# Performance work log

Hardware: AMD Instinct MI355X
Metric: run time of the kernel (lower is better)

Reference implementation:

```python
import jax, jax.numpy as jnp
import numpy as np
from jax import lax

L_TAU = 0.8
NUM_TIME = 20
B, H, W = 128, 64, 64
FLAT = 6 * 27 * 27  # 4374 features after conv(k=10)->55x55 and maxpool2 -> 27x27

def setup_inputs() -> dict:
    key = jax.random.key(0)
    k1, k2, k3, k4, k5, k6 = jax.random.split(key, 6)
    x = jax.random.uniform(k1, (B, H * W, NUM_TIME), dtype=jnp.float32)
    y = jax.random.randint(k2, (B,), 0, 2, dtype=jnp.int64)
    Wc = jax.random.normal(k3, (6, 1, 10, 10), dtype=jnp.float32) * 0.1  # OIHW
    bc = jnp.zeros((6,), dtype=jnp.float32)
    W2 = jax.random.normal(k4, (FLAT, 2), dtype=jnp.float32) * (1.0 / np.sqrt(FLAT))
    b2 = jnp.zeros((2,), dtype=jnp.float32)
    return {"x": x, "y": y, "Wc": Wc, "bc": bc, "W2": W2, "b2": b2}

def _maxpool2(a):
    return lax.reduce_window(a, -jnp.inf, lax.max,
                             (1, 1, 2, 2), (1, 1, 2, 2), 'VALID')

def _snu_forward(x, Wc, bc, W2, b2):
    xt = jnp.transpose(x, (2, 0, 1)).reshape(NUM_TIME, B, 1, H, W)  # [T,B,1,64,64]
    s1 = jnp.zeros((B, 6, 55, 55), jnp.float32); y1 = jnp.zeros_like(s1)
    s2 = jnp.zeros((B, 2), jnp.float32);        y2 = jnp.zeros_like(s2)

    def step(carry, x_t):
        s1, y1, s2, y2 = carry
        c = lax.conv_general_dilated(x_t, Wc, (1, 1), 'VALID',
                                     dimension_numbers=('NCHW', 'OIHW', 'NCHW'))
        # SNU state: s = relu(conv(x) + l_tau * s * (1 - y)); emission: y = sigmoid(s + b)
        s1 = jax.nn.relu(c + L_TAU * s1 * (1.0 - y1))
        y1 = jax.nn.sigmoid(s1 + bc[None, :, None, None])
        h = _maxpool2(y1).reshape(B, FLAT)           # [B, 4374]
        s2 = jax.nn.relu(h @ W2 + L_TAU * s2 * (1.0 - y2))
        y2 = jax.nn.sigmoid(s2 + b2)
        return (s1, y1, s2, y2), y2

    _, outs = lax.scan(step, (s1, y1, s2, y2), xt)   # [T, B, 2]
    out_rec = jnp.concatenate([jnp.zeros((1, B, 2), jnp.float32), outs], axis=0)
    out_rec = jnp.transpose(out_rec, (1, 0, 2))      # [B, T+1, 2]
    m = jnp.sum(out_rec, axis=1) / 20.0
    return m, out_rec

def reference(x, y, Wc, bc, W2, b2):
    m, out_rec = _snu_forward(x, Wc, bc, W2, b2)
    logp = jax.nn.log_softmax(m, axis=1)
    loss = -jnp.mean(logp[jnp.arange(B), y])         # CrossEntropyLoss
    acc = jnp.mean((jnp.argmax(m, axis=1) == y).astype(jnp.float32))
    return (loss, m, out_rec, acc)
```

## Files before the change

kernel.cpp:

```cpp
#include <hip/hip_runtime.h>
#include <hip/hip_bf16.h>
#include <math.h>

#define L_TAU_C 0.8f

typedef _Float16 half2_t __attribute__((ext_vector_type(2)));

union U32H2 { unsigned int u; half2_t h; };
__device__ __forceinline__ half2_t h2(unsigned int v) { U32H2 x; x.u = v; return x.h; }

__device__ __forceinline__ float sigmoidf_(float x) {
    return 1.0f / (1.0f + __expf(-x));
}

__global__ __launch_bounds__(256) void k_transpose16(const float* __restrict__ x,
                                                     _Float16* __restrict__ xT) {
    int gp = blockIdx.x * 256 + threadIdx.x;
    int b = gp >> 12, p = gp & 4095;
    const float4* src = reinterpret_cast<const float4*>(x + (size_t)gp * 20);
    float v[20];
#pragma unroll
    for (int k = 0; k < 5; ++k) {
        float4 q = src[k];
        v[4 * k + 0] = q.x; v[4 * k + 1] = q.y; v[4 * k + 2] = q.z; v[4 * k + 3] = q.w;
    }
    _Float16* dst = xT + (size_t)b * 20 * 4096 + p;
#pragma unroll
    for (int t = 0; t < 20; ++t) dst[(size_t)t * 4096] = (_Float16)v[t];
}

template<int XMODE>
__global__ __launch_bounds__(192, 4) void k_conv_snu(
    const float* __restrict__ x,
    const _Float16* __restrict__ xT,
    const float* __restrict__ Wc,
    const float* __restrict__ bc,
    const float* __restrict__ W2,
    float* __restrict__ partw)
{
    const int tid = threadIdx.x;
    const int bi = blockIdx.x;
    const int xcd = bi & 7, slot = bi >> 3;
    const int b = (slot / 6) * 8 + xcd;
    const int ch = slot % 6;

    const bool active = tid < 189;
    const int r = tid / 7;
    const int g = tid % 7;
    const int row0 = 2 * r;

    const float* wb = Wc + ch * 100;
    unsigned int wsg[50];
#pragma unroll
    for (int i = 0; i < 50; ++i) {
        U32H2 pk;
        pk.h = half2_t{(_Float16)wb[2 * i], (_Float16)wb[2 * i + 1]};
        wsg[i] = (unsigned int)__builtin_amdgcn_readfirstlane((int)pk.u);
    }

    float s1[2][8], y1[2][8];
#pragma unroll
    for (int i = 0; i < 2; ++i)
#pragma unroll
        for (int j = 0; j < 8; ++j) { s1[i][j] = 0.f; y1[i][j] = 0.f; }

    const float bch = bc[ch];

    float w2r[4][2];
#pragma unroll
    for (int pj = 0; pj < 4; ++pj) { w2r[pj][0] = 0.f; w2r[pj][1] = 0.f; }
    if (active) {
#pragma unroll
        for (int pj = 0; pj < 4; ++pj) {
            int pc = 4 * g + pj;
            if (pc < 27) {
                int f0 = ch * 729 + r * 27 + pc;
                w2r[pj][0] = W2[(size_t)f0 * 2 + 0];
                w2r[pj][1] = W2[(size_t)f0 * 2 + 1];
            }
        }
    }

    const _Float16* xb16 = xT + (size_t)b * 20 * 4096;
    const float* xb32 = x + (size_t)b * 4096 * 20;
    const int off17 = (g < 6) ? 16 : 14;

    for (int t = 0; t < 20; ++t) {
        float p0 = 0.f, p1 = 0.f;
        if (active) {
            float c0[8], c1[8];
#pragma unroll
            for (int j = 0; j < 8; ++j) { c0[j] = 0.f; c1[j] = 0.f; }

#pragma unroll
            for (int xr = 0; xr < 11; ++xr) {
                const int R = row0 + xr;
                unsigned int s[9];
                if (XMODE == 1) {
                    const _Float16* rp = xb16 + (size_t)t * 4096 + R * 64 + 8 * g;
                    uint4 A = *reinterpret_cast<const uint4*>(rp);
                    uint4 B = *reinterpret_cast<const uint4*>(rp + 8);
                    unsigned int C = *reinterpret_cast<const unsigned int*>(rp + off17);
                    s[0] = A.x; s[1] = A.y; s[2] = A.z; s[3] = A.w;
                    s[4] = B.x; s[5] = B.y; s[6] = B.z; s[7] = B.w;
                    s[8] = C;
                } else {
                    const float* rp = xb32 + ((size_t)R * 64 + 8 * g) * 20 + t;
#pragma unroll
                    for (int q = 0; q < 8; ++q) {
                        U32H2 pk;
                        pk.h = half2_t{(_Float16)rp[(2 * q) * 20],
                                       (_Float16)rp[(2 * q + 1) * 20]};
                        s[q] = pk.u;
                    }
                    {
                        U32H2 pk;
                        pk.h = half2_t{(_Float16)rp[off17 * 20],
                                       (_Float16)rp[(off17 + 1) * 20]};
                        s[8] = pk.u;
                    }
                }
                unsigned int ss[8];
#pragma unroll
                for (int i = 0; i < 8; ++i)
                    ss[i] = (s[i] >> 16) | (s[i + 1] << 16);

                if (xr <= 9) {
#pragma unroll
                    for (int m = 0; m < 5; ++m) {
                        half2_t w = h2(wsg[xr * 5 + m]);
                        c0[0] = __builtin_amdgcn_fdot2(h2(s[m]),      w, c0[0], false);
                        c0[1] = __builtin_amdgcn_fdot2(h2(ss[m]),     w, c0[1], false);
                        c0[2] = __builtin_amdgcn_fdot2(h2(s[m + 1]),  w, c0[2], false);
                        c0[3] = __builtin_amdgcn_fdot2(h2(ss[m + 1]), w, c0[3], false);
                        c0[4] = __builtin_amdgcn_fdot2(h2(s[m + 2]),  w, c0[4], false);
                        c0[5] = __builtin_amdgcn_fdot2(h2(ss[m + 2]), w, c0[5], false);
                        c0[6] = __builtin_amdgcn_fdot2(h2(s[m + 3]),  w, c0[6], false);
                        c0[7] = __builtin_amdgcn_fdot2(h2(ss[m + 3]), w, c0[7], false);
                    }
                }
                if (xr >= 1) {
#pragma unroll
                    for (int m = 0; m < 5; ++m) {
                        half2_t w = h2(wsg[(xr - 1) * 5 + m]);
                        c1[0] = __builtin_amdgcn_fdot2(h2(s[m]),      w, c1[0], false);
                        c1[1] = __builtin_amdgcn_fdot2(h2(ss[m]),     w, c1[1], false);
                        c1[2] = __builtin_amdgcn_fdot2(h2(s[m + 1]),  w, c1[2], false);
                        c1[3] = __builtin_amdgcn_fdot2(h2(ss[m + 1]), w, c1[3], false);
                        c1[4] = __builtin_amdgcn_fdot2(h2(s[m + 2]),  w, c1[4], false);
                        c1[5] = __builtin_amdgcn_fdot2(h2(ss[m + 2]), w, c1[5], false);
                        c1[6] = __builtin_amdgcn_fdot2(h2(s[m + 3]),  w, c1[6], false);
                        c1[7] = __builtin_amdgcn_fdot2(h2(ss[m + 3]), w, c1[7], false);
                    }
                }
            }
#pragma unroll
            for (int j = 0; j < 8; ++j) {
                float sa = fmaxf(c0[j] + L_TAU_C * s1[0][j] * (1.f - y1[0][j]), 0.f);
                float sb = fmaxf(c1[j] + L_TAU_C * s1[1][j] * (1.f - y1[1][j]), 0.f);
                s1[0][j] = sa; s1[1][j] = sb;
                y1[0][j] = sigmoidf_(sa + bch);
                y1[1][j] = sigmoidf_(sb + bch);
            }
#pragma unroll
            for (int pj = 0; pj < 4; ++pj) {
                float h = fmaxf(fmaxf(y1[0][2 * pj], y1[0][2 * pj + 1]),
                                fmaxf(y1[1][2 * pj], y1[1][2 * pj + 1]));
                p0 += h * w2r[pj][0];
                p1 += h * w2r[pj][1];
            }
        }
#pragma unroll
        for (int off = 32; off >= 1; off >>= 1) {
            p0 += __shfl_down(p0, off);
            p1 += __shfl_down(p1, off);
        }
        if ((tid & 63) == 0) {
            float2 val; val.x = p0; val.y = p1;
            *reinterpret_cast<float2*>(
                &partw[((((size_t)t * 128 + b) * 6 + ch) * 3 + (tid >> 6)) * 2]) = val;
        }
    }
}

__global__ __launch_bounds__(128) void k_final(const float* __restrict__ partw,
                                               const void* __restrict__ yraw,
                                               const float* __restrict__ b2,
                                               float* __restrict__ out) {
    __shared__ float red[4];
    const int b = threadIdx.x;

    const int* yi = (const int*)yraw;
    bool i64 = true;
    for (int k = 0; k < 64; ++k) {
        if (yi[2 * k + 1] != 0) { i64 = false; break; }
    }
    int lbl = i64 ? (int)((const long long*)yraw)[b] : yi[b];

    float b20 = b2[0], b21 = b2[1];
    float s20 = 0.f, s21 = 0.f, y20 = 0.f, y21 = 0.f, m0 = 0.f, m1 = 0.f;
    float* orec = out + 257 + b * 42;
    orec[0] = 0.f; orec[1] = 0.f;
    for (int t = 0; t < 20; ++t) {
        const float4* pp = reinterpret_cast<const float4*>(
            partw + ((size_t)t * 128 + b) * 36);
        float sum0 = 0.f, sum1 = 0.f;
#pragma unroll
        for (int i = 0; i < 9; ++i) {
            float4 a = pp[i];
            sum0 += a.x + a.z;
            sum1 += a.y + a.w;
        }
        s20 = fmaxf(sum0 + L_TAU_C * s20 * (1.f - y20), 0.f);
        s21 = fmaxf(sum1 + L_TAU_C * s21 * (1.f - y21), 0.f);
        y20 = sigmoidf_(s20 + b20);
        y21 = sigmoidf_(s21 + b21);
        orec[(t + 1) * 2 + 0] = y20;
        orec[(t + 1) * 2 + 1] = y21;
        m0 += y20; m1 += y21;
    }
    m0 *= 0.05f; m1 *= 0.05f;
    out[1 + b * 2 + 0] = m0;
    out[1 + b * 2 + 1] = m1;

    float mx = fmaxf(m0, m1);
    float lse = mx + logf(expf(m0 - mx) + expf(m1 - mx));
    float lossc = -(((lbl != 0) ? m1 : m0) - lse);
    int pred = (m1 > m0) ? 1 : 0;
    float accc = (pred == lbl) ? 1.f : 0.f;
#pragma unroll
    for (int off = 32; off >= 1; off >>= 1) {
        lossc += __shfl_down(lossc, off);
        accc += __shfl_down(accc, off);
    }
    if ((b & 63) == 0) { red[(b >> 6) * 2] = lossc; red[(b >> 6) * 2 + 1] = accc; }
    __syncthreads();
    if (b == 0) {
        out[0] = (red[0] + red[2]) * (1.f / 128.f);
        out[5633] = (red[1] + red[3]) * (1.f / 128.f);
    }
}

extern "C" void kernel_launch(void* const* d_in, const int* in_sizes, int n_in,
                              void* d_out, int out_size, void* d_ws, size_t ws_size,
                              hipStream_t stream) {
    const float* x  = (const float*)d_in[0];
    const void*  y  = d_in[1];
    const float* Wc = (const float*)d_in[2];
    const float* bc = (const float*)d_in[3];
    const float* W2 = (const float*)d_in[4];
    const float* b2 = (const float*)d_in[5];
    float* out = (float*)d_out;

    const size_t xt_bytes = (size_t)128 * 20 * 4096 * 2;
    const size_t partw_bytes = (size_t)20 * 128 * 6 * 3 * 2 * 4;
    const int use16 = (ws_size >= xt_bytes + partw_bytes) ? 1 : 0;

    _Float16* xT = (_Float16*)d_ws;
    float* partw = use16 ? (float*)((char*)d_ws + xt_bytes) : (float*)d_ws;

    if (use16) {
        k_transpose16<<<2048, 256, 0, stream>>>(x, xT);
        k_conv_snu<1><<<768, 192, 0, stream>>>(x, xT, Wc, bc, W2, partw);
    } else {
        k_conv_snu<0><<<768, 192, 0, stream>>>(x, (const _Float16*)d_ws, Wc, bc, W2, partw);
    }
    k_final<<<1, 128, 0, stream>>>(partw, y, b2, out);
}
```

Before: 178.4 us.

## Halve per-thread conv tile to double threads per block in conv SNU kernel

Each thread now computes a 2x4 conv output tile (two pooled columns) instead of 2x8, so blocks grow from 192 to 384 threads and the partial-sum buffer doubles to six wave slots per channel. The aim is more parallelism and lower register pressure per thread, which improves latency hiding. In exchange, overlapping input rows are loaded redundantly across more threads, with more shuffle reductions and more partials for the final kernel to sum.

Result: faster. 159.9 us (-10.4%).

```diff
diff --git a/kernel.cpp b/kernel.cpp
--- a/kernel.cpp
+++ b/kernel.cpp
@@ -30,7 +30,7 @@
 }
 
 template<int XMODE>
-__global__ __launch_bounds__(192, 4) void k_conv_snu(
+__global__ __launch_bounds__(384, 2) void k_conv_snu(
     const float* __restrict__ x,
     const _Float16* __restrict__ xT,
     const float* __restrict__ Wc,
@@ -44,9 +44,9 @@
     const int b = (slot / 6) * 8 + xcd;
     const int ch = slot % 6;
 
-    const bool active = tid < 189;
-    const int r = tid / 7;
-    const int g = tid % 7;
+    const bool active = tid < 378;
+    const int r = tid / 14;
+    const int pcg = tid % 14;
     const int row0 = 2 * r;
 
     const float* wb = Wc + ch * 100;
@@ -58,71 +58,62 @@
         wsg[i] = (unsigned int)__builtin_amdgcn_readfirstlane((int)pk.u);
     }
 
-    float s1[2][8], y1[2][8];
+    float s1[2][4], y1[2][4];
 #pragma unroll
     for (int i = 0; i < 2; ++i)
 #pragma unroll
-        for (int j = 0; j < 8; ++j) { s1[i][j] = 0.f; y1[i][j] = 0.f; }
+        for (int j = 0; j < 4; ++j) { s1[i][j] = 0.f; y1[i][j] = 0.f; }
 
     const float bch = bc[ch];
 
-    float w2r[4][2];
-#pragma unroll
-    for (int pj = 0; pj < 4; ++pj) { w2r[pj][0] = 0.f; w2r[pj][1] = 0.f; }
+    float w2r[2][2];
+    w2r[0][0] = 0.f; w2r[0][1] = 0.f; w2r[1][0] = 0.f; w2r[1][1] = 0.f;
     if (active) {
 #pragma unroll
-        for (int pj = 0; pj < 4; ++pj) {
-            int pc = 4 * g + pj;
+        for (int k = 0; k < 2; ++k) {
+            int pc = 2 * pcg + k;
             if (pc < 27) {
                 int f0 = ch * 729 + r * 27 + pc;
-                w2r[pj][0] = W2[(size_t)f0 * 2 + 0];
-                w2r[pj][1] = W2[(size_t)f0 * 2 + 1];
+                w2r[k][0] = W2[(size_t)f0 * 2 + 0];
+                w2r[k][1] = W2[(size_t)f0 * 2 + 1];
             }
         }
     }
 
     const _Float16* xb16 = xT + (size_t)b * 20 * 4096;
     const float* xb32 = x + (size_t)b * 4096 * 20;
-    const int off17 = (g < 6) ? 16 : 14;
 
     for (int t = 0; t < 20; ++t) {
         float p0 = 0.f, p1 = 0.f;
         if (active) {
-            float c0[8], c1[8];
-#pragma unroll
-            for (int j = 0; j < 8; ++j) { c0[j] = 0.f; c1[j] = 0.f; }
+            float c0[4] = {0.f, 0.f, 0.f, 0.f};
+            float c1[4] = {0.f, 0.f, 0.f, 0.f};
 
 #pragma unroll
             for (int xr = 0; xr < 11; ++xr) {
                 const int R = row0 + xr;
-                unsigned int s[9];
+                unsigned int s[7];
                 if (XMODE == 1) {
-                    const _Float16* rp = xb16 + (size_t)t * 4096 + R * 64 + 8 * g;
-                    uint4 A = *reinterpret_cast<const uint4*>(rp);
-                    uint4 B = *reinterpret_cast<const uint4*>(rp + 8);
-                    unsigned int C = *reinterpret_cast<const unsigned int*>(rp + off17);
-                    s[0] = A.x; s[1] = A.y; s[2] = A.z; s[3] = A.w;
-                    s[4] = B.x; s[5] = B.y; s[6] = B.z; s[7] = B.w;
-                    s[8] = C;
+                    const _Float16* rp = xb16 + (size_t)t * 4096 + R * 64 + 4 * pcg;
+                    uint2 a = *reinterpret_cast<const uint2*>(rp);
+                    uint2 bq = *reinterpret_cast<const uint2*>(rp + 4);
+                    uint2 cq = *reinterpret_cast<const uint2*>(rp + 8);
+                    unsigned int dq = *reinterpret_cast<const unsigned int*>(rp + 12);
+                    s[0] = a.x; s[1] = a.y; s[2] = bq.x; s[3] = bq.y;
+                    s[4] = cq.x; s[5] = cq.y; s[6] = dq;
                 } else {
-                    const float* rp = xb32 + ((size_t)R * 64 + 8 * g) * 20 + t;
-#pragma unroll
-                    for (int q = 0; q < 8; ++q) {
+                    const float* rp = xb32 + ((size_t)R * 64 + 4 * pcg) * 20 + t;
+#pragma unroll
+                    for (int q = 0; q < 7; ++q) {
                         U32H2 pk;
                         pk.h = half2_t{(_Float16)rp[(2 * q) * 20],
                                        (_Float16)rp[(2 * q + 1) * 20]};
                         s[q] = pk.u;
                     }
-                    {
-                        U32H2 pk;
-                        pk.h = half2_t{(_Float16)rp[off17 * 20],
-                                       (_Float16)rp[(off17 + 1) * 20]};
-                        s[8] = pk.u;
-                    }
                 }
-                unsigned int ss[8];
-#pragma unroll
-                for (int i = 0; i < 8; ++i)
+                unsigned int ss[6];
+#pragma unroll
+                for (int i = 0; i < 6; ++i)
                     ss[i] = (s[i] >> 16) | (s[i + 1] << 16);
 
                 if (xr <= 9) {
@@ -133,10 +124,6 @@
                         c0[1] = __builtin_amdgcn_fdot2(h2(ss[m]),     w, c0[1], false);
                         c0[2] = __builtin_amdgcn_fdot2(h2(s[m + 1]),  w, c0[2], false);
                         c0[3] = __builtin_amdgcn_fdot2(h2(ss[m + 1]), w, c0[3], false);
-                        c0[4] = __builtin_amdgcn_fdot2(h2(s[m + 2]),  w, c0[4], false);
-                        c0[5] = __builtin_amdgcn_fdot2(h2(ss[m + 2]), w, c0[5], false);
-                        c0[6] = __builtin_amdgcn_fdot2(h2(s[m + 3]),  w, c0[6], false);
-                        c0[7] = __builtin_amdgcn_fdot2(h2(ss[m + 3]), w, c0[7], false);
                     }
                 }
                 if (xr >= 1) {
@@ -147,28 +134,21 @@
                         c1[1] = __builtin_amdgcn_fdot2(h2(ss[m]),     w, c1[1], false);
                         c1[2] = __builtin_amdgcn_fdot2(h2(s[m + 1]),  w, c1[2], false);
                         c1[3] = __builtin_amdgcn_fdot2(h2(ss[m + 1]), w, c1[3], false);
-                        c1[4] = __builtin_amdgcn_fdot2(h2(s[m + 2]),  w, c1[4], false);
-                        c1[5] = __builtin_amdgcn_fdot2(h2(ss[m + 2]), w, c1[5], false);
-                        c1[6] = __builtin_amdgcn_fdot2(h2(s[m + 3]),  w, c1[6], false);
-                        c1[7] = __builtin_amdgcn_fdot2(h2(ss[m + 3]), w, c1[7], false);
                     }
                 }
             }
 #pragma unroll
-            for (int j = 0; j < 8; ++j) {
+            for (int j = 0; j < 4; ++j) {
                 float sa = fmaxf(c0[j] + L_TAU_C * s1[0][j] * (1.f - y1[0][j]), 0.f);
                 float sb = fmaxf(c1[j] + L_TAU_C * s1[1][j] * (1.f - y1[1][j]), 0.f);
                 s1[0][j] = sa; s1[1][j] = sb;
                 y1[0][j] = sigmoidf_(sa + bch);
                 y1[1][j] = sigmoidf_(sb + bch);
             }
-#pragma unroll
-            for (int pj = 0; pj < 4; ++pj) {
-                float h = fmaxf(fmaxf(y1[0][2 * pj], y1[0][2 * pj + 1]),
-                                fmaxf(y1[1][2 * pj], y1[1][2 * pj + 1]));
-                p0 += h * w2r[pj][0];
-                p1 += h * w2r[pj][1];
-            }
+            float h0 = fmaxf(fmaxf(y1[0][0], y1[0][1]), fmaxf(y1[1][0], y1[1][1]));
+            float h1 = fmaxf(fmaxf(y1[0][2], y1[0][3]), fmaxf(y1[1][2], y1[1][3]));
+            p0 = h0 * w2r[0][0] + h1 * w2r[1][0];
+            p1 = h0 * w2r[0][1] + h1 * w2r[1][1];
         }
 #pragma unroll
         for (int off = 32; off >= 1; off >>= 1) {
@@ -178,7 +158,7 @@
         if ((tid & 63) == 0) {
             float2 val; val.x = p0; val.y = p1;
             *reinterpret_cast<float2*>(
-                &partw[((((size_t)t * 128 + b) * 6 + ch) * 3 + (tid >> 6)) * 2]) = val;
+                &partw[((((size_t)t * 128 + b) * 6 + ch) * 6 + (tid >> 6)) * 2]) = val;
         }
     }
 }
@@ -203,10 +183,10 @@
     orec[0] = 0.f; orec[1] = 0.f;
     for (int t = 0; t < 20; ++t) {
         const float4* pp = reinterpret_cast<const float4*>(
-            partw + ((size_t)t * 128 + b) * 36);
+            partw + ((size_t)t * 128 + b) * 72);
         float sum0 = 0.f, sum1 = 0.f;
 #pragma unroll
-        for (int i = 0; i < 9; ++i) {
+        for (int i = 0; i < 18; ++i) {
             float4 a = pp[i];
             sum0 += a.x + a.z;
             sum1 += a.y + a.w;
@@ -253,7 +233,7 @@
     float* out = (float*)d_out;
 
     const size_t xt_bytes = (size_t)128 * 20 * 4096 * 2;
-    const size_t partw_bytes = (size_t)20 * 128 * 6 * 3 * 2 * 4;
+    const size_t partw_bytes = (size_t)20 * 128 * 6 * 6 * 2 * 4;
     const int use16 = (ws_size >= xt_bytes + partw_bytes) ? 1 : 0;
 
     _Float16* xT = (_Float16*)d_ws;
@@ -261,9 +241,9 @@
 
     if (use16) {
         k_transpose16<<<2048, 256, 0, stream>>>(x, xT);
-        k_conv_snu<1><<<768, 192, 0, stream>>>(x, xT, Wc, bc, W2, partw);
+        k_conv_snu<1><<<768, 384, 0, stream>>>(x, xT, Wc, bc, W2, partw);
     } else {
-        k_conv_snu<0><<<768, 192, 0, stream>>>(x, (const _Float16*)d_ws, Wc, bc, W2, partw);
+        k_conv_snu<0><<<768, 384, 0, stream>>>(x, (const _Float16*)d_ws, Wc, bc, W2, partw);
     }
     k_final<<<1, 128, 0, stream>>>(partw, y, b2, out);
 }
```
